# Kernel optimization log

Measured on AMD Instinct MI355X. Metric: run time of the kernel, lower is better.

## Reference

```python
import math
import jax, jax.numpy as jnp
import numpy as np

S, D, E = 8192, 2048, 64            # tokens, model_dim, num_experts
CAPACITY_FACTOR = 1.0
CAP = int(CAPACITY_FACTOR * math.ceil(S / E))  # 128, static (training-mode 'drop' gate)


def setup_inputs() -> dict:
    key = jax.random.key(0)
    kx, kw = jax.random.split(key)
    x = jax.random.normal(kx, (S, D), dtype=jnp.float32)
    wg = jax.random.normal(kw, (E, D), dtype=jnp.float32) * 0.02  # Linear(D, E, bias=False) weight
    return {"x": x, "wg": wg}


def reference(x, wg):
    # logits = self.wg(input)
    logits = jnp.einsum('sd,ed->se', x, wg)                 # [S, E]
    gates = jax.nn.softmax(logits, axis=1)                  # [S, E]
    indices1_s = jnp.argmax(gates, axis=1)                  # [S]
    mask1 = jax.nn.one_hot(indices1_s, E, dtype=gates.dtype)  # [S, E]

    # load-balancing aux loss
    me = jnp.mean(gates, axis=0)
    ce = jnp.mean(mask1, axis=0)
    l_aux = jnp.mean(me * ce) * (E * E)

    # gates1_s computed BEFORE capacity drop (as in source)
    gates1_s = jnp.sum(gates * mask1, axis=1)               # [S]

    # fused_cumsum_sub_one: position of each token within its expert's queue
    locations1 = jnp.cumsum(mask1, axis=0) - 1.0            # [S, E]
    # capacity drop ('drop' gate type)
    mask1 = mask1 * (locations1 < CAP).astype(mask1.dtype)
    locations1_s = jnp.sum(locations1 * mask1, axis=1).astype(jnp.int32)  # [S]

    gates1 = gates1_s[:, None] * mask1                      # [S, E]
    locations1_sc = jax.nn.one_hot(locations1_s, CAP, dtype=gates1.dtype)  # [S, CAP]
    # bmm(gates1[:,:,None], loc_sc[:,None,:]) == outer product per token
    combine1_sec = jnp.einsum('se,sc->sec', gates1, locations1_sc)  # [S, E, CAP]
    dispatch_mask = combine1_sec.astype(bool)
    return l_aux, combine1_sec, dispatch_mask
```

## Files before the change

### kernel.cpp

```cpp
#include <hip/hip_runtime.h>
#include <cstddef>
#include <cstdint>

#define S_TOK 8192
#define DDIM  2048
#define NEXP  64
#define CAPTY 128
#define KC    64
#define TPB   64
#define NBLK  (S_TOK / TPB)
#define SPLITK 8
#define KPER  (DDIM / SPLITK)
#define SEC   ((size_t)S_TOK * NEXP * CAPTY)

__global__ __launch_bounds__(256)
void gate_gemm_kernel(const float* __restrict__ x, const float* __restrict__ wg,
                      float* __restrict__ part)
{
    __shared__ float xs[TPB][72];
    __shared__ float ws[KC][NEXP];

    const int tid = threadIdx.x;
    const int el  = tid & 15;
    const int tg  = tid >> 4;
    const int kp  = blockIdx.x & (SPLITK - 1);
    const int tc  = blockIdx.x >> 3;
    const int t_base = tc * TPB;
    const int k_base = kp * KPER;

    float acc[4][4];
#pragma unroll
    for (int i = 0; i < 4; ++i)
#pragma unroll
        for (int j = 0; j < 4; ++j) acc[i][j] = 0.0f;

    for (int kc0 = 0; kc0 < KPER; kc0 += KC) {
        const int kc = k_base + kc0;
        __syncthreads();
#pragma unroll
        for (int m = 0; m < 4; ++m) {
            int idx = tid + 256 * m;
            int t = idx >> 4;
            int c = idx & 15;
            float4 v = *(const float4*)(x + (size_t)(t_base + t) * DDIM + kc + c * 4);
            *(float4*)&xs[t][c * 4] = v;
        }
#pragma unroll
        for (int m = 0; m < 4; ++m) {
            int idx = tid + 256 * m;
            int e = idx & 63;
            int c = idx >> 6;
            float4 w = *(const float4*)(wg + (size_t)e * DDIM + kc + c * 4);
            ws[c * 4 + 0][e] = w.x;
            ws[c * 4 + 1][e] = w.y;
            ws[c * 4 + 2][e] = w.z;
            ws[c * 4 + 3][e] = w.w;
        }
        __syncthreads();

#pragma unroll
        for (int k4 = 0; k4 < KC; k4 += 4) {
            float4 xv[4], wv[4];
#pragma unroll
            for (int i = 0; i < 4; ++i)
                xv[i] = *(const float4*)&xs[tg + 16 * i][k4];
#pragma unroll
            for (int j = 0; j < 4; ++j)
                wv[j] = *(const float4*)&ws[k4 + j][el * 4];
#pragma unroll
            for (int i = 0; i < 4; ++i) {
                acc[i][0] += xv[i].x * wv[0].x; acc[i][1] += xv[i].x * wv[0].y;
                acc[i][2] += xv[i].x * wv[0].z; acc[i][3] += xv[i].x * wv[0].w;
                acc[i][0] += xv[i].y * wv[1].x; acc[i][1] += xv[i].y * wv[1].y;
                acc[i][2] += xv[i].y * wv[1].z; acc[i][3] += xv[i].y * wv[1].w;
                acc[i][0] += xv[i].z * wv[2].x; acc[i][1] += xv[i].z * wv[2].y;
                acc[i][2] += xv[i].z * wv[2].z; acc[i][3] += xv[i].z * wv[2].w;
                acc[i][0] += xv[i].w * wv[3].x; acc[i][1] += xv[i].w * wv[3].y;
                acc[i][2] += xv[i].w * wv[3].z; acc[i][3] += xv[i].w * wv[3].w;
            }
        }
    }

#pragma unroll
    for (int i = 0; i < 4; ++i) {
        int t = tg + 16 * i;
        float4 v = make_float4(acc[i][0], acc[i][1], acc[i][2], acc[i][3]);
        *(float4*)(part + ((size_t)kp * S_TOK + t_base + t) * NEXP + el * 4) = v;
    }
}

__global__ __launch_bounds__(256)
void softmax_kernel(const float* __restrict__ part,
                    float* __restrict__ gate_s, int* __restrict__ expert,
                    int* __restrict__ rank, int* __restrict__ hist,
                    float* __restrict__ partial_g)
{
    __shared__ float probs[TPB][NEXP + 1];
    __shared__ int   sexp[TPB];

    const int tid = threadIdx.x;
    const int t_base = blockIdx.x * TPB;
    const int t = tid >> 2, q = tid & 3;
    const int tok = t_base + t;

#pragma unroll
    for (int jj = 0; jj < 4; ++jj) {
        float4 a = make_float4(0.f, 0.f, 0.f, 0.f);
#pragma unroll
        for (int kpp = 0; kpp < SPLITK; ++kpp) {
            float4 v = *(const float4*)(part + ((size_t)kpp * S_TOK + tok) * NEXP + q * 16 + jj * 4);
            a.x += v.x; a.y += v.y; a.z += v.z; a.w += v.w;
        }
        probs[t][q * 16 + jj * 4 + 0] = a.x;
        probs[t][q * 16 + jj * 4 + 1] = a.y;
        probs[t][q * 16 + jj * 4 + 2] = a.z;
        probs[t][q * 16 + jj * 4 + 3] = a.w;
    }
    __syncthreads();

    if (tid < TPB) {
        const int t2 = tid, tok2 = t_base + t2;
        float m = -1e30f; int am = 0;
        for (int e = 0; e < NEXP; ++e) {
            float v = probs[t2][e];
            if (v > m) { m = v; am = e; }
        }
        float s = 0.0f;
        for (int e = 0; e < NEXP; ++e) s += __expf(probs[t2][e] - m);
        float rcp = 1.0f / s;
        for (int e = 0; e < NEXP; ++e)
            probs[t2][e] = __expf(probs[t2][e] - m) * rcp;
        sexp[t2] = am;
        gate_s[tok2] = rcp;
        expert[tok2] = am;
    }
    __syncthreads();

    if (tid < TPB) {
        const int t2 = tid;
        const int am = sexp[t2];
        int r = 0;
        for (int u = 0; u < t2; ++u) r += (sexp[u] == am) ? 1 : 0;
        rank[t_base + t2] = r;
    } else if (tid < 2 * TPB) {
        const int e = tid - TPB;
        float pg = 0.0f; int cnt = 0;
        for (int u = 0; u < TPB; ++u) {
            pg  += probs[u][e];
            cnt += (sexp[u] == e) ? 1 : 0;
        }
        partial_g[blockIdx.x * NEXP + e] = pg;
        hist[blockIdx.x * NEXP + e]      = cnt;
    }
}

__global__ __launch_bounds__(64)
void scan_kernel(const int* __restrict__ hist, const float* __restrict__ partial_g,
                 int* __restrict__ chunk_base, float* __restrict__ l_aux_ws)
{
    int e = threadIdx.x;
    int base = 0;
    float sg = 0.0f;
    for (int c = 0; c < NBLK; ++c) {
        chunk_base[c * NEXP + e] = base;
        base += hist[c * NEXP + e];
        sg   += partial_g[c * NEXP + e];
    }
    float v = sg * (float)base;
#pragma unroll
    for (int off = 32; off > 0; off >>= 1) v += __shfl_down(v, off);
    if (e == 0)
        l_aux_ws[0] = v * (64.0f / (8192.0f * 8192.0f));
}

__global__ __launch_bounds__(256)
void scatter_kernel(const float* __restrict__ gate_s, const int* __restrict__ expert,
                    const int* __restrict__ rank, const int* __restrict__ chunk_base,
                    const float* __restrict__ l_aux_ws, float* __restrict__ out)
{
    int s = blockIdx.x * 256 + threadIdx.x;
    if (s == 0) out[0] = l_aux_ws[0];
    if (s >= S_TOK) return;
    int e   = expert[s];
    int loc = chunk_base[(s >> 6) * NEXP + e] + rank[s];
    if (loc < CAPTY) {
        size_t idx = 1 + (size_t)s * (NEXP * CAPTY) + (size_t)e * CAPTY + loc;
        out[idx]       = gate_s[s];
        out[idx + SEC] = 1.0f;
    }
}

extern "C" void kernel_launch(void* const* d_in, const int* in_sizes, int n_in,
                              void* d_out, int out_size, void* d_ws, size_t ws_size,
                              hipStream_t stream)
{
    const float* x  = (const float*)d_in[0];
    const float* wg = (const float*)d_in[1];
    float* out = (float*)d_out;
    char* ws = (char*)d_ws;

    float* part      = (float*)(ws + 0);
    size_t off = (size_t)SPLITK * S_TOK * NEXP * sizeof(float);
    float* gate_s    = (float*)(ws + off);          off += 32768;
    int*   expert    = (int*)  (ws + off);          off += 32768;
    int*   rank      = (int*)  (ws + off);          off += 32768;
    int*   hist      = (int*)  (ws + off);          off += 32768;
    float* partial_g = (float*)(ws + off);          off += 32768;
    int*   chunk_b   = (int*)  (ws + off);          off += 32768;
    float* l_aux_ws  = (float*)(ws + off);

    gate_gemm_kernel<<<NBLK * SPLITK, 256, 0, stream>>>(x, wg, part);
    softmax_kernel<<<NBLK, 256, 0, stream>>>(part, gate_s, expert, rank, hist, partial_g);
    scan_kernel<<<1, 64, 0, stream>>>(hist, partial_g, chunk_b, l_aux_ws);

    hipMemsetAsync(d_out, 0, (size_t)(1 + 2 * SEC) * sizeof(float), stream);

    scatter_kernel<<<(S_TOK + 255) / 256, 256, 0, stream>>>(gate_s, expert, rank,
                                                            chunk_b, l_aux_ws, out);
}
```

Baseline: 593.8 us.

## Fuse output zero-fill into gate GEMM kernel with nontemporal stores

```diff
diff --git a/kernel.cpp b/kernel.cpp
--- a/kernel.cpp
+++ b/kernel.cpp
@@ -12,19 +12,39 @@
 #define SPLITK 8
 #define KPER  (DDIM / SPLITK)
 #define SEC   ((size_t)S_TOK * NEXP * CAPTY)
+#define NOUT  (1 + 2 * SEC)
+#define F4_FILLONLY 24576
+#define F4_GEMM     8192
+
+typedef float f32x4 __attribute__((ext_vector_type(4)));
 
 __global__ __launch_bounds__(256)
-void gate_gemm_kernel(const float* __restrict__ x, const float* __restrict__ wg,
-                      float* __restrict__ part)
+void fill_gemm_kernel(const float* __restrict__ x, const float* __restrict__ wg,
+                      float* __restrict__ part, float* __restrict__ out)
 {
     __shared__ float xs[TPB][72];
     __shared__ float ws[KC][NEXP];
 
     const int tid = threadIdx.x;
+    const int b   = blockIdx.x;
+    f32x4* __restrict__ out4 = (f32x4*)out;
+    const f32x4 z4 = {0.f, 0.f, 0.f, 0.f};
+
+    if ((b & 1) == 0) {
+        const int f = b >> 1;
+        size_t base = (size_t)f * F4_FILLONLY + tid;
+#pragma unroll 8
+        for (int j = 0; j < F4_FILLONLY / 256; ++j)
+            __builtin_nontemporal_store(z4, &out4[base + (size_t)j * 256]);
+        if (b == 0 && tid == 0) out[NOUT - 1] = 0.0f;
+        return;
+    }
+
+    const int g   = b >> 1;
     const int el  = tid & 15;
     const int tg  = tid >> 4;
-    const int kp  = blockIdx.x & (SPLITK - 1);
-    const int tc  = blockIdx.x >> 3;
+    const int kp  = g & (SPLITK - 1);
+    const int tc  = g >> 3;
     const int t_base = tc * TPB;
     const int k_base = kp * KPER;
 
@@ -87,6 +107,11 @@
         float4 v = make_float4(acc[i][0], acc[i][1], acc[i][2], acc[i][3]);
         *(float4*)(part + ((size_t)kp * S_TOK + t_base + t) * NEXP + el * 4) = v;
     }
+
+    size_t base = (size_t)1024 * F4_FILLONLY + (size_t)g * F4_GEMM + tid;
+#pragma unroll 8
+    for (int j = 0; j < F4_GEMM / 256; ++j)
+        __builtin_nontemporal_store(z4, &out4[base + (size_t)j * 256]);
 }
 
 __global__ __launch_bounds__(256)
@@ -209,12 +234,9 @@
     int*   chunk_b   = (int*)  (ws + off);          off += 32768;
     float* l_aux_ws  = (float*)(ws + off);
 
-    gate_gemm_kernel<<<NBLK * SPLITK, 256, 0, stream>>>(x, wg, part);
+    fill_gemm_kernel<<<2048, 256, 0, stream>>>(x, wg, part, out);
     softmax_kernel<<<NBLK, 256, 0, stream>>>(part, gate_s, expert, rank, hist, partial_g);
     scan_kernel<<<1, 64, 0, stream>>>(hist, partial_g, chunk_b, l_aux_ws);
-
-    hipMemsetAsync(d_out, 0, (size_t)(1 + 2 * SEC) * sizeof(float), stream);
-
     scatter_kernel<<<(S_TOK + 255) / 256, 256, 0, stream>>>(gate_s, expert, rank,
                                                             chunk_b, l_aux_ws, out);
 }
```

New measurement: 615.8 us. +3.7%, slower.

## Pre-transpose gate weights and compute all 64 experts per thread in gate GEMM

Applied to the files above, without the earlier changes.

```diff
diff --git a/kernel.cpp b/kernel.cpp
--- a/kernel.cpp
+++ b/kernel.cpp
@@ -12,81 +12,82 @@
 #define SPLITK 8
 #define KPER  (DDIM / SPLITK)
 #define SEC   ((size_t)S_TOK * NEXP * CAPTY)
+#define NOUT  ((size_t)1 + 2 * SEC)
+#define WGT_OFF ((size_t)1 << 28)
 
 __global__ __launch_bounds__(256)
-void gate_gemm_kernel(const float* __restrict__ x, const float* __restrict__ wg,
+void wg_transpose_kernel(const float* __restrict__ wg, float* __restrict__ wgT)
+{
+    __shared__ float tile[64][65];
+    const int kt  = blockIdx.x;
+    const int tid = threadIdx.x;
+#pragma unroll
+    for (int m = 0; m < 4; ++m) {
+        int idx = tid + 256 * m;
+        int e = idx >> 4, c = idx & 15;
+        float4 v = *(const float4*)(wg + (size_t)e * DDIM + kt * 64 + c * 4);
+        tile[c * 4 + 0][e] = v.x;
+        tile[c * 4 + 1][e] = v.y;
+        tile[c * 4 + 2][e] = v.z;
+        tile[c * 4 + 3][e] = v.w;
+    }
+    __syncthreads();
+#pragma unroll
+    for (int m = 0; m < 4; ++m) {
+        int idx = tid + 256 * m;
+        int k = idx >> 4, c = idx & 15;
+        float4 v = make_float4(tile[k][c * 4 + 0], tile[k][c * 4 + 1],
+                               tile[k][c * 4 + 2], tile[k][c * 4 + 3]);
+        *(float4*)(wgT + (size_t)(kt * 64 + k) * NEXP + c * 4) = v;
+    }
+}
+
+__global__ __launch_bounds__(64)
+void gate_gemm_kernel(const float* __restrict__ x, const float* __restrict__ wgT,
                       float* __restrict__ part)
 {
-    __shared__ float xs[TPB][72];
-    __shared__ float ws[KC][NEXP];
-
-    const int tid = threadIdx.x;
-    const int el  = tid & 15;
-    const int tg  = tid >> 4;
-    const int kp  = blockIdx.x & (SPLITK - 1);
-    const int tc  = blockIdx.x >> 3;
+    __shared__ float xs[KC][TPB + 1];
+
+    const int lane = threadIdx.x;
+    const int kp   = blockIdx.x & (SPLITK - 1);
+    const int tc   = blockIdx.x >> 3;
     const int t_base = tc * TPB;
     const int k_base = kp * KPER;
 
-    float acc[4][4];
-#pragma unroll
-    for (int i = 0; i < 4; ++i)
-#pragma unroll
-        for (int j = 0; j < 4; ++j) acc[i][j] = 0.0f;
+    float acc[NEXP];
+#pragma unroll
+    for (int e = 0; e < NEXP; ++e) acc[e] = 0.0f;
 
     for (int kc0 = 0; kc0 < KPER; kc0 += KC) {
         const int kc = k_base + kc0;
-        __syncthreads();
-#pragma unroll
-        for (int m = 0; m < 4; ++m) {
-            int idx = tid + 256 * m;
+#pragma unroll
+        for (int m = 0; m < 16; ++m) {
+            int idx = lane + 64 * m;
             int t = idx >> 4;
             int c = idx & 15;
             float4 v = *(const float4*)(x + (size_t)(t_base + t) * DDIM + kc + c * 4);
-            *(float4*)&xs[t][c * 4] = v;
-        }
-#pragma unroll
-        for (int m = 0; m < 4; ++m) {
-            int idx = tid + 256 * m;
-            int e = idx & 63;
-            int c = idx >> 6;
-            float4 w = *(const float4*)(wg + (size_t)e * DDIM + kc + c * 4);
-            ws[c * 4 + 0][e] = w.x;
-            ws[c * 4 + 1][e] = w.y;
-            ws[c * 4 + 2][e] = w.z;
-            ws[c * 4 + 3][e] = w.w;
-        }
-        __syncthreads();
-
-#pragma unroll
-        for (int k4 = 0; k4 < KC; k4 += 4) {
-            float4 xv[4], wv[4];
-#pragma unroll
-            for (int i = 0; i < 4; ++i)
-                xv[i] = *(const float4*)&xs[tg + 16 * i][k4];
-#pragma unroll
-            for (int j = 0; j < 4; ++j)
-                wv[j] = *(const float4*)&ws[k4 + j][el * 4];
-#pragma unroll
-            for (int i = 0; i < 4; ++i) {
-                acc[i][0] += xv[i].x * wv[0].x; acc[i][1] += xv[i].x * wv[0].y;
-                acc[i][2] += xv[i].x * wv[0].z; acc[i][3] += xv[i].x * wv[0].w;
-                acc[i][0] += xv[i].y * wv[1].x; acc[i][1] += xv[i].y * wv[1].y;
-                acc[i][2] += xv[i].y * wv[1].z; acc[i][3] += xv[i].y * wv[1].w;
-                acc[i][0] += xv[i].z * wv[2].x; acc[i][1] += xv[i].z * wv[2].y;
-                acc[i][2] += xv[i].z * wv[2].z; acc[i][3] += xv[i].z * wv[2].w;
-                acc[i][0] += xv[i].w * wv[3].x; acc[i][1] += xv[i].w * wv[3].y;
-                acc[i][2] += xv[i].w * wv[3].z; acc[i][3] += xv[i].w * wv[3].w;
-            }
-        }
-    }
-
-#pragma unroll
-    for (int i = 0; i < 4; ++i) {
-        int t = tg + 16 * i;
-        float4 v = make_float4(acc[i][0], acc[i][1], acc[i][2], acc[i][3]);
-        *(float4*)(part + ((size_t)kp * S_TOK + t_base + t) * NEXP + el * 4) = v;
-    }
+            xs[c * 4 + 0][t] = v.x;
+            xs[c * 4 + 1][t] = v.y;
+            xs[c * 4 + 2][t] = v.z;
+            xs[c * 4 + 3][t] = v.w;
+        }
+
+        const float* __restrict__ wrow = wgT + (size_t)kc * NEXP;
+#pragma unroll 2
+        for (int k = 0; k < KC; ++k) {
+            float xk = xs[k][lane];
+            const float* __restrict__ wk = wrow + k * NEXP;
+#pragma unroll
+            for (int e = 0; e < NEXP; ++e)
+                acc[e] += xk * wk[e];
+        }
+    }
+
+    float* p = part + ((size_t)kp * S_TOK + t_base + lane) * NEXP;
+#pragma unroll
+    for (int e4 = 0; e4 < 16; ++e4)
+        *(float4*)(p + e4 * 4) = make_float4(acc[e4 * 4 + 0], acc[e4 * 4 + 1],
+                                             acc[e4 * 4 + 2], acc[e4 * 4 + 3]);
 }
 
 __global__ __launch_bounds__(256)
@@ -209,12 +210,13 @@
     int*   chunk_b   = (int*)  (ws + off);          off += 32768;
     float* l_aux_ws  = (float*)(ws + off);
 
-    gate_gemm_kernel<<<NBLK * SPLITK, 256, 0, stream>>>(x, wg, part);
+    float* wgT = out + WGT_OFF;
+
+    wg_transpose_kernel<<<DDIM / 64, 256, 0, stream>>>(wg, wgT);
+    gate_gemm_kernel<<<NBLK * SPLITK, 64, 0, stream>>>(x, wgT, part);
     softmax_kernel<<<NBLK, 256, 0, stream>>>(part, gate_s, expert, rank, hist, partial_g);
     scan_kernel<<<1, 64, 0, stream>>>(hist, partial_g, chunk_b, l_aux_ws);
-
-    hipMemsetAsync(d_out, 0, (size_t)(1 + 2 * SEC) * sizeof(float), stream);
-
+    hipMemsetAsync(d_out, 0, NOUT * sizeof(float), stream);
     scatter_kernel<<<(S_TOK + 255) / 256, 256, 0, stream>>>(gate_s, expert, rank,
                                                             chunk_b, l_aux_ws, out);
 }
```

Measured after the change: 670.4 us. 1.13x slower.
